# Kernel optimization log

Hardware: AMD Instinct MI355X
Metric: run time of the kernel (lower is better)

## Reference

```python
import jax, jax.numpy as jnp
import numpy as np

HID = 4544; NH = 71; NKV = 1; HD = 64  # Falcon-7B MQA geometry (head_dim hardcoded 64 in _split_heads)
B = 1; U = 32; C = 4; S = 2048          # batch, users, kv chunks, chunk length


def rotate_half(x):
    d = x.shape[-1] // 2
    return jnp.concatenate((-x[..., d:], x[..., :d]), axis=-1)


def setup_inputs() -> dict:
    key = jax.random.key(0)
    ks = jax.random.split(key, 7)
    hidden_states = jax.random.normal(ks[0], (B, U, HID), jnp.float32)
    cos = jax.random.uniform(ks[1], (1, U, 1, HD), jnp.float32, -1.0, 1.0)
    sin = jax.random.uniform(ks[2], (1, U, 1, HD), jnp.float32, -1.0, 1.0)
    k_cache = jax.random.normal(ks[3], (C, B, U, S, HD), jnp.float32)
    v_cache = jax.random.normal(ks[4], (C, B, U, S, HD), jnp.float32)
    attn_masks = jnp.zeros((C, B, U, S), jnp.float32)
    w_qkv = jax.random.normal(ks[5], ((NKV * (NH // NKV + 2)) * HD, HID), jnp.float32) * 0.02
    w_dense = jax.random.normal(ks[6], (HID, HID), jnp.float32) * 0.02
    return {"hidden_states": hidden_states, "cos": cos, "sin": sin,
            "k_cache": k_cache, "v_cache": v_cache, "attn_masks": attn_masks,
            "w_qkv": w_qkv, "w_dense": w_dense}


def reference(hidden_states, cos, sin, k_cache, v_cache, attn_masks, w_qkv, w_dense):
    b, u, _ = hidden_states.shape
    # fused QKV projection (Linear without bias: x @ W.T)
    fused = hidden_states @ w_qkv.T                      # [b,u,(NH+2*NKV)*HD]
    qkv = fused.reshape(b, u, NKV, NH // NKV + 2, HD)    # _split_heads view
    q = qkv[:, :, :, :-2].reshape(b, u, NH, HD)          # query heads
    k_cur = qkv[:, :, :, -2].reshape(b, u, NKV, HD)      # shared MQA key head
    v_cur = qkv[:, :, :, -1].reshape(b, u, NKV, HD)      # shared MQA value head
    # rotary embedding (apply_rotary_pos_emb)
    q = q * cos + rotate_half(q) * sin
    k_cur = k_cur * cos + rotate_half(k_cur) * sin
    inv = 1.0 / jnp.sqrt(jnp.float32(HD))
    # flash-decode over cached chunks: scores [c,b,u,n,s]
    scores = jnp.einsum('bund,cbusd->cbuns', q, k_cache) * inv
    scores = scores + attn_masks[:, :, :, None, :]
    m_c = jnp.max(scores, axis=-1, keepdims=True)        # [c,b,u,n,1] local max
    p = jnp.exp(scores - m_c)
    l_c = jnp.sum(p, axis=-1, keepdims=True)             # local row sums
    # current token = length-1 chunk (its local max is itself, local sum is 1)
    s_cur = jnp.einsum('bund,bued->bune', q, k_cur) * inv  # [b,u,n,1]
    g = jnp.maximum(jnp.max(m_c, axis=0), s_cur)           # global max [b,u,n,1]
    factor = jnp.exp(m_c - g[None])                        # per-chunk rescale
    out = jnp.einsum('cbuns,cbusd->bund', factor * p, v_cache)
    cur_w = jnp.exp(s_cur - g)                             # [b,u,n,1]
    out = out + cur_w * v_cur                              # v_cur broadcasts over heads
    scale = jnp.sum(factor * l_c, axis=0) + cur_w
    out = out / scale
    attn = out.reshape(b, u, NH * HD)
    return attn @ w_dense.T
```

## Files before the change

### kernel.cpp

```cpp
#include <hip/hip_runtime.h>
#include <hip/hip_bf16.h>

typedef __bf16 bf16_t;
typedef __bf16 bf16x8 __attribute__((ext_vector_type(8)));
typedef float  f32x4  __attribute__((ext_vector_type(4)));

#define MFMA16(A,B,C) __builtin_amdgcn_mfma_f32_16x16x32_bf16(A,B,C,0,0,0)

constexpr int HIDc = 4544;
constexpr int NHc  = 71;
constexpr int NHPc = 80;
constexpr int HDc  = 64;
constexpr int Uc   = 32;
constexpr int Sc   = 2048;
constexpr int RQ   = 4672;

constexpr size_t OFF_FUSED = 0;
constexpr size_t OFF_QHI   = 598016;
constexpr size_t OFF_QLO   = 925696;
constexpr size_t OFF_KCUR  = 1253376;
constexpr size_t OFF_VCUR  = 1261568;
constexpr size_t OFF_MP    = 1269760;
constexpr size_t OFF_LP    = 1415168;
constexpr size_t OFF_AHI   = 1560576;
constexpr size_t OFF_ALO   = 1851392;
constexpr size_t OFF_OP    = 2142208;

__device__ __forceinline__ bf16x8 ld8f(const float* base, long eidx) {
  const float* p = base + eidx;
  const f32x4 a = *(const f32x4*)p;
  const f32x4 b = *(const f32x4*)(p + 4);
  bf16x8 r;
  r[0]=(bf16_t)a[0]; r[1]=(bf16_t)a[1]; r[2]=(bf16_t)a[2]; r[3]=(bf16_t)a[3];
  r[4]=(bf16_t)b[0]; r[5]=(bf16_t)b[1]; r[6]=(bf16_t)b[2]; r[7]=(bf16_t)b[3];
  return r;
}

__device__ __forceinline__ void cp16(const float* g, float* l) {
  __builtin_amdgcn_global_load_lds((const __attribute__((address_space(1))) void*)g,
                                   (__attribute__((address_space(3))) void*)l, 16, 0, 0);
}
__device__ __forceinline__ void cp4(const float* g, float* l) {
  __builtin_amdgcn_global_load_lds((const __attribute__((address_space(1))) void*)g,
                                   (__attribute__((address_space(3))) void*)l, 4, 0, 0);
}

__global__ __launch_bounds__(256) void k_zeros(float* fused, float* out) {
  const int i = blockIdx.x*256 + threadIdx.x;
  if (i < Uc*RQ) fused[i] = 0.f;
  else           out[i - Uc*RQ] = 0.f;
}

__global__ __launch_bounds__(256) void k_qkv(
    const float* __restrict__ hidden, const float* __restrict__ wqkv,
    float* __restrict__ fused)
{
  const int h = blockIdx.x, y = blockIdx.y;
  const int t = threadIdx.x;
  const int wave = t >> 6, lane = t & 63;
  const int c = lane & 15, q4 = lane >> 4;
  const int mt = wave & 1, kh = wave >> 1;
  const int ks0 = y*18;
  const int ksn = min(18, 142 - ks0);
  const int h1  = ksn >> 1;
  const int kbeg = ks0 + (kh ? h1 : 0);
  const int kend = ks0 + (kh ? ksn : h1);
  __shared__ float sD[Uc*HDc];

  const long abase = (long)(mt*16 + c)*HIDc + q4*8;
  const long bbase = ((long)h*64 + c)*HIDc + q4*8;
  f32x4 acc[4] = {};
#pragma unroll 3
  for (int ks = kbeg; ks < kend; ++ks) {
    const bf16x8 af = ld8f(hidden, abase + ks*32);
#pragma unroll
    for (int nf = 0; nf < 4; ++nf) {
      const bf16x8 bv = ld8f(wqkv, bbase + (long)nf*16*HIDc + ks*32);
      acc[nf] = MFMA16(af, bv, acc[nf]);
    }
  }
  if (kh == 0) {
#pragma unroll
    for (int r = 0; r < 4; ++r)
#pragma unroll
      for (int nf = 0; nf < 4; ++nf)
        sD[(mt*16 + q4*4 + r)*64 + nf*16 + c] = acc[nf][r];
  }
  __syncthreads();
  if (kh == 1) {
#pragma unroll
    for (int r = 0; r < 4; ++r)
#pragma unroll
      for (int nf = 0; nf < 4; ++nf)
        sD[(mt*16 + q4*4 + r)*64 + nf*16 + c] += acc[nf][r];
  }
  __syncthreads();
  for (int i = t; i < Uc*HDc; i += 256)
    atomicAdd(&fused[(long)(i >> 6)*RQ + h*64 + (i & 63)], sD[i]);
}

__global__ __launch_bounds__(256) void k_rotary(
    const float* __restrict__ fused,
    const float* __restrict__ cosp, const float* __restrict__ sinp,
    bf16_t* __restrict__ qhi, bf16_t* __restrict__ qlo,
    float* __restrict__ kcur, float* __restrict__ vcur)
{
  const int h = blockIdx.x;
  const int t = threadIdx.x;
  __shared__ float sD[Uc*HDc];
  if (h < 73) {
    for (int i = t; i < Uc*HDc; i += 256)
      sD[i] = fused[(long)(i >> 6)*RQ + h*64 + (i & 63)];
    __syncthreads();
  }
  if (h >= NHc) {
    for (int i = t; i < Uc*HDc; i += 256) {
      const long idx = (((long)(i >> 6))*NHPc + h)*HDc + (i & 63);
      qhi[idx] = (bf16_t)0.f;  qlo[idx] = (bf16_t)0.f;
    }
  }
  if (h >= 73) return;
  for (int i = t; i < Uc*HDc; i += 256) {
    const int u = i >> 6, d = i & 63;
    const float x = sD[i];
    const float partner = sD[i ^ 32];
    const float cs = cosp[u*HDc + d];
    const float sn = sinp[u*HDc + d];
    const float rh = (d < 32) ? -partner : partner;
    const float val = x*cs + rh*sn;
    if (h < NHc) {
      const long idx = ((long)u*NHPc + h)*HDc + d;
      const bf16_t hi = (bf16_t)val;
      qhi[idx] = hi;
      qlo[idx] = (bf16_t)(val - (float)hi);
    } else if (h == NHc) {
      kcur[u*HDc + d] = val;
    } else {
      vcur[u*HDc + d] = x;
    }
  }
}

constexpr int ATTN_SMEM_FLOATS = 35456;
constexpr int ATTN_SMEM_BYTES  = ATTN_SMEM_FLOATS * 4;

__global__ __launch_bounds__(256, 1) void k_attn(
    const float* __restrict__ kc, const float* __restrict__ vc,
    const float* __restrict__ masks,
    const bf16_t* __restrict__ qhi, const bf16_t* __restrict__ qlo,
    float* __restrict__ Mp, float* __restrict__ Lp, float* __restrict__ Op,
    const int NPB)
{
  extern __shared__ float smem[];
  const int u  = blockIdx.x;
  const int pb = blockIdx.y;
  const int tid = threadIdx.x;
  const int wave = __builtin_amdgcn_readfirstlane(tid >> 6);
  const int lane = tid & 63;
  const int c    = lane & 15;
  const int q4   = lane >> 4;
  const int pbpc = NPB >> 2;
  const int keys_pb   = 2048 / pbpc;
  const int keys_wave = keys_pb >> 2;
  const int tcnt      = keys_wave >> 5;
  const int chunk = pb / pbpc;
  const int inner = pb - chunk*pbpc;
  const int s_base = inner*keys_pb + wave*keys_wave;
  const long kvbase = ((long)(chunk*Uc + u))*Sc;

  float* const wstage = smem + wave*8192;
  float* const mwave  = smem + 32768 + wave*512;
  float* const sM     = smem + 34816;
  float* const sL     = smem + 35136;
  float* const sO     = smem;

  const int srow = lane >> 4;
  const int scol = (lane & 15) << 2;

  {
    const long tb = (kvbase + s_base) * 64;
    const float* gK = kc + tb;
    const float* gV = vc + tb;
#pragma unroll
    for (int i = 0; i < 8; ++i) {
      const int row = i*4 + srow;
      const int fz = ((row & 7) << 2) ^ (((row >> 3) & 1) << 4);
      const int off = row*64 + (scol ^ fz);
      cp16(gK + off, wstage + i*256);
      cp16(gV + off, wstage + 2048 + i*256);
    }
    const int nmc = keys_wave >> 6;
    const float* gM = masks + kvbase + s_base;
    for (int i = 0; i < nmc; ++i)
      cp4(gM + i*64 + lane, mwave + i*64);
  }

  bf16x8 qh[5][2], ql[5][2];
  const bf16_t* qb  = qhi + ((long)u*NHPc + c)*HDc + q4*8;
  const bf16_t* qb2 = qlo + ((long)u*NHPc + c)*HDc + q4*8;
#pragma unroll
  for (int ht = 0; ht < 5; ++ht)
#pragma unroll
    for (int ks = 0; ks < 2; ++ks) {
      qh[ht][ks] = *(const bf16x8*)(qb  + ht*16*HDc + ks*32);
      ql[ht][ks] = *(const bf16x8*)(qb2 + ht*16*HDc + ks*32);
    }

  float m_i[5], l_i[5];
  f32x4 Oa[5][4] = {};
#pragma unroll
  for (int ht = 0; ht < 5; ++ht) { m_i[ht] = -INFINITY; l_i[ht] = 0.f; }

  const int krow0 = ((c >> 2) << 3) + (c & 3);

  for (int t = 0; t < tcnt; ++t) {
    float* const lK = wstage + (t & 1)*4096;
    float* const lV = lK + 2048;

    if (t + 1 < tcnt) {
      float* const nK = wstage + ((t+1) & 1)*4096;
      const long tb = (kvbase + s_base + (long)(t+1)*32) * 64;
      const float* gK = kc + tb;
      const float* gV = vc + tb;
#pragma unroll
      for (int i = 0; i < 8; ++i) {
        const int row = i*4 + srow;
        const int fz = ((row & 7) << 2) ^ (((row >> 3) & 1) << 4);
        const int off = row*64 + (scol ^ fz);
        cp16(gK + off, nK + i*256);
        cp16(gV + off, nK + 2048 + i*256);
      }
      asm volatile("s_waitcnt vmcnt(16)" ::: "memory");
    } else {
      asm volatile("s_waitcnt vmcnt(0)" ::: "memory");
    }
    __builtin_amdgcn_sched_barrier(0);

    bf16x8 kf[2][2];
#pragma unroll
    for (int mt2 = 0; mt2 < 2; ++mt2) {
      const int row = krow0 + mt2*4;
      const int fz = ((row & 7) << 2) ^ (((row >> 3) & 1) << 4);
#pragma unroll
      for (int ks = 0; ks < 2; ++ks) {
        const int b0 = row*64 + ((ks*32 + q4*8) ^ fz);
        const int b1 = row*64 + ((ks*32 + q4*8 + 4) ^ fz);
        const f32x4 a = *(const f32x4*)(lK + b0);
        const f32x4 b = *(const f32x4*)(lK + b1);
        bf16x8 r;
        r[0]=(bf16_t)a[0]; r[1]=(bf16_t)a[1]; r[2]=(bf16_t)a[2]; r[3]=(bf16_t)a[3];
        r[4]=(bf16_t)b[0]; r[5]=(bf16_t)b[1]; r[6]=(bf16_t)b[2]; r[7]=(bf16_t)b[3];
        kf[mt2][ks] = r;
      }
    }

    bf16x8 vf[4];
#pragma unroll
    for (int dt = 0; dt < 4; ++dt) {
      union { bf16_t e[8]; bf16x8 v; } uv;
#pragma unroll
      for (int j = 0; j < 8; ++j) {
        const int row = q4*8 + j;
        const int fz = ((row & 7) << 2) ^ (((row >> 3) & 1) << 4);
        uv.e[j] = (bf16_t)lV[row*64 + ((dt*16 + c) ^ fz)];
      }
      vf[dt] = uv.v;
    }

    f32x4 S[2][5];
#pragma unroll
    for (int mt2 = 0; mt2 < 2; ++mt2)
#pragma unroll
      for (int ht = 0; ht < 5; ++ht) {
        f32x4 s = {};
        s = MFMA16(kf[mt2][0], qh[ht][0], s);
        s = MFMA16(kf[mt2][1], qh[ht][1], s);
        s = MFMA16(kf[mt2][0], ql[ht][0], s);
        s = MFMA16(kf[mt2][1], ql[ht][1], s);
        S[mt2][ht] = s;
      }

    float mk[2][4];
#pragma unroll
    for (int mt2 = 0; mt2 < 2; ++mt2)
#pragma unroll
      for (int r = 0; r < 4; ++r)
        mk[mt2][r] = mwave[t*32 + q4*8 + mt2*4 + r];
#pragma unroll
    for (int mt2 = 0; mt2 < 2; ++mt2)
#pragma unroll
      for (int ht = 0; ht < 5; ++ht)
#pragma unroll
        for (int r = 0; r < 4; ++r)
          S[mt2][ht][r] = S[mt2][ht][r]*0.125f + mk[mt2][r];

    float alpha[5];
#pragma unroll
    for (int ht = 0; ht < 5; ++ht) {
      float tm = S[0][ht][0];
#pragma unroll
      for (int mt2 = 0; mt2 < 2; ++mt2)
#pragma unroll
        for (int r = 0; r < 4; ++r) tm = fmaxf(tm, S[mt2][ht][r]);
      tm = fmaxf(tm, __shfl_xor(tm, 16));
      tm = fmaxf(tm, __shfl_xor(tm, 32));
      const float mn = fmaxf(m_i[ht], tm);
      alpha[ht] = __expf(m_i[ht] - mn);
      m_i[ht] = mn;
    }
#pragma unroll
    for (int mt2 = 0; mt2 < 2; ++mt2)
#pragma unroll
      for (int ht = 0; ht < 5; ++ht)
#pragma unroll
        for (int r = 0; r < 4; ++r)
          S[mt2][ht][r] = __expf(S[mt2][ht][r] - m_i[ht]);
#pragma unroll
    for (int ht = 0; ht < 5; ++ht) {
      float rs = 0.f;
#pragma unroll
      for (int mt2 = 0; mt2 < 2; ++mt2)
#pragma unroll
        for (int r = 0; r < 4; ++r) rs += S[mt2][ht][r];
      rs += __shfl_xor(rs, 16);
      rs += __shfl_xor(rs, 32);
      l_i[ht] = l_i[ht]*alpha[ht] + rs;
    }
#pragma unroll
    for (int ht = 0; ht < 5; ++ht)
#pragma unroll
      for (int r = 0; r < 4; ++r) {
        const float ar = __shfl(alpha[ht], q4*4 + r);
#pragma unroll
        for (int dt = 0; dt < 4; ++dt) Oa[ht][dt][r] *= ar;
      }
    bf16x8 ph[5], pl[5];
#pragma unroll
    for (int ht = 0; ht < 5; ++ht) {
      union { bf16_t e[8]; bf16x8 v; } uh, ul;
#pragma unroll
      for (int j = 0; j < 8; ++j) {
        const float val = (j < 4) ? S[0][ht][j] : S[1][ht][j & 3];
        const bf16_t hi = (bf16_t)val;
        uh.e[j] = hi;
        ul.e[j] = (bf16_t)(val - (float)hi);
      }
      ph[ht] = uh.v;  pl[ht] = ul.v;
    }
#pragma unroll
    for (int ht = 0; ht < 5; ++ht)
#pragma unroll
      for (int dt = 0; dt < 4; ++dt) {
        Oa[ht][dt] = MFMA16(ph[ht], vf[dt], Oa[ht][dt]);
        Oa[ht][dt] = MFMA16(pl[ht], vf[dt], Oa[ht][dt]);
      }
  }

  if (lane < 16)
#pragma unroll
    for (int ht = 0; ht < 5; ++ht) {
      sM[wave*80 + ht*16 + lane] = m_i[ht];
      sL[wave*80 + ht*16 + lane] = l_i[ht];
    }
  __syncthreads();
#pragma unroll
  for (int ht = 0; ht < 5; ++ht)
#pragma unroll
    for (int r = 0; r < 4; ++r) {
      const int hh = ht*16 + q4*4 + r;
      float mg = fmaxf(fmaxf(sM[hh], sM[80 + hh]), fmaxf(sM[160 + hh], sM[240 + hh]));
      mg = fmaxf(mg, -1e30f);
      const float aw = __expf(sM[wave*80 + hh] - mg);
#pragma unroll
      for (int dt = 0; dt < 4; ++dt) Oa[ht][dt][r] *= aw;
    }
  for (int w = 0; w < 4; ++w) {
    if (wave == w) {
#pragma unroll
      for (int ht = 0; ht < 5; ++ht)
#pragma unroll
        for (int dt = 0; dt < 4; ++dt)
#pragma unroll
          for (int r = 0; r < 4; ++r) {
            const int idx = (ht*16 + q4*4 + r)*HDc + dt*16 + c;
            if (w == 0) sO[idx] = Oa[ht][dt][r];
            else        sO[idx] += Oa[ht][dt][r];
          }
    }
    __syncthreads();
  }
  float* op = Op + ((long)u*NPB + pb)*NHc*HDc;
  for (int i = tid; i < NHc*HDc; i += 256) op[i] = sO[i];
  if (wave == 0 && lane < 16) {
#pragma unroll
    for (int ht = 0; ht < 5; ++ht) {
      const int hh = ht*16 + lane;
      if (hh < NHc) {
        float mg = fmaxf(fmaxf(sM[hh], sM[80 + hh]), fmaxf(sM[160 + hh], sM[240 + hh]));
        mg = fmaxf(mg, -1e30f);
        float L = 0.f;
#pragma unroll
        for (int w = 0; w < 4; ++w) L += __expf(sM[w*80 + hh] - mg)*sL[w*80 + hh];
        Mp[((long)u*NPB + pb)*NHc + hh] = mg;
        Lp[((long)u*NPB + pb)*NHc + hh] = L;
      }
    }
  }
}

__global__ __launch_bounds__(64) void k_combine(
    const float* __restrict__ Mp, const float* __restrict__ Lp,
    const float* __restrict__ Op,
    const bf16_t* __restrict__ qhi, const bf16_t* __restrict__ qlo,
    const float* __restrict__ kcur, const float* __restrict__ vcur,
    bf16_t* __restrict__ ahi, bf16_t* __restrict__ alo, const int NPB)
{
  const int h = blockIdx.x, u = blockIdx.y;
  const int lane = threadIdx.x;
  const long qidx = ((long)u*NHPc + h)*HDc + lane;
  float pr = ((float)qhi[qidx] + (float)qlo[qidx]) * kcur[u*HDc + lane];
#pragma unroll
  for (int o = 32; o > 0; o >>= 1) pr += __shfl_xor(pr, o);
  const float s_cur = pr * 0.125f;

  float g = s_cur;
  for (int p = 0; p < NPB; ++p)
    g = fmaxf(g, Mp[((long)u*NPB + p)*NHc + h]);
  g = fmaxf(g, -1e30f);
  float sw = 0.f, acc = 0.f;
  const float* ob = Op + (long)u*NPB*NHc*HDc + (long)h*HDc + lane;
  for (int p = 0; p < NPB; ++p) {
    const float f = __expf(Mp[((long)u*NPB + p)*NHc + h] - g);
    sw += f*Lp[((long)u*NPB + p)*NHc + h];
    acc += f*ob[(long)p*NHc*HDc];
  }
  const float cw = __expf(s_cur - g);
  acc += cw * vcur[u*HDc + lane];
  const float attn = acc / (sw + cw);
  const bf16_t hi = (bf16_t)attn;
  ahi[(long)u*HIDc + h*HDc + lane] = hi;
  alo[(long)u*HIDc + h*HDc + lane] = (bf16_t)(attn - (float)hi);
}

__global__ __launch_bounds__(256) void k_outgemm(
    const bf16_t* __restrict__ ahi, const bf16_t* __restrict__ alo,
    const float* __restrict__ wd, float* __restrict__ out)
{
  const int nb = blockIdx.x, y = blockIdx.y;
  const int t = threadIdx.x;
  const int wave = t >> 6, lane = t & 63;
  const int c = lane & 15, q4 = lane >> 4;
  const int mt = wave & 1, kh = wave >> 1;
  const int ks0 = y*18;
  const int ksn = min(18, 142 - ks0);
  const int h1  = ksn >> 1;
  const int kbeg = ks0 + (kh ? h1 : 0);
  const int kend = ks0 + (kh ? ksn : h1);
  __shared__ float sC[Uc*32];

  const bf16_t* aph = ahi + ((long)(mt*16 + c))*HIDc + q4*8;
  const bf16_t* apl = alo + ((long)(mt*16 + c))*HIDc + q4*8;
  const long bbase = ((long)nb*32 + c)*HIDc + q4*8;

  f32x4 acc[2] = {};
#pragma unroll 3
  for (int ks = kbeg; ks < kend; ++ks) {
    const bf16x8 Ah = *(const bf16x8*)(aph + ks*32);
    const bf16x8 Al = *(const bf16x8*)(apl + ks*32);
#pragma unroll
    for (int nf = 0; nf < 2; ++nf) {
      const bf16x8 B = ld8f(wd, bbase + (long)nf*16*HIDc + ks*32);
      acc[nf] = MFMA16(Ah, B, acc[nf]);
      acc[nf] = MFMA16(Al, B, acc[nf]);
    }
  }
  if (kh == 0) {
#pragma unroll
    for (int r = 0; r < 4; ++r)
#pragma unroll
      for (int nf = 0; nf < 2; ++nf)
        sC[(mt*16 + q4*4 + r)*32 + nf*16 + c] = acc[nf][r];
  }
  __syncthreads();
  if (kh == 1) {
#pragma unroll
    for (int r = 0; r < 4; ++r)
#pragma unroll
      for (int nf = 0; nf < 2; ++nf)
        sC[(mt*16 + q4*4 + r)*32 + nf*16 + c] += acc[nf][r];
  }
  __syncthreads();
  for (int i = t; i < Uc*32; i += 256)
    atomicAdd(&out[(long)(i >> 5)*HIDc + nb*32 + (i & 31)], sC[i]);
}

extern "C" void kernel_launch(void* const* d_in, const int* in_sizes, int n_in,
                              void* d_out, int out_size, void* d_ws, size_t ws_size,
                              hipStream_t stream)
{
  const float* hidden = (const float*)d_in[0];
  const float* cosp   = (const float*)d_in[1];
  const float* sinp   = (const float*)d_in[2];
  const float* kcache = (const float*)d_in[3];
  const float* vcache = (const float*)d_in[4];
  const float* masks  = (const float*)d_in[5];
  const float* wqkv   = (const float*)d_in[6];
  const float* wdense = (const float*)d_in[7];
  float* out = (float*)d_out;

  const size_t opb = (size_t)Uc*NHc*HDc*4;
  int NPB = 16;
  if      (ws_size >= OFF_OP + 16*opb) NPB = 16;
  else if (ws_size >= OFF_OP +  8*opb) NPB = 8;
  else if (ws_size >= OFF_OP +  4*opb) NPB = 4;
  else return;

  char* ws = (char*)d_ws;
  float*  fused = (float*)(ws + OFF_FUSED);
  bf16_t* qhi   = (bf16_t*)(ws + OFF_QHI);
  bf16_t* qlo   = (bf16_t*)(ws + OFF_QLO);
  float*  kcur  = (float*)(ws + OFF_KCUR);
  float*  vcur  = (float*)(ws + OFF_VCUR);
  float*  Mp    = (float*)(ws + OFF_MP);
  float*  Lp    = (float*)(ws + OFF_LP);
  bf16_t* ahi   = (bf16_t*)(ws + OFF_AHI);
  bf16_t* alo   = (bf16_t*)(ws + OFF_ALO);
  float*  Op    = (float*)(ws + OFF_OP);

  hipFuncSetAttribute(reinterpret_cast<const void*>(k_attn),
                      hipFuncAttributeMaxDynamicSharedMemorySize, ATTN_SMEM_BYTES);

  k_zeros  <<<1152, 256, 0, stream>>>(fused, out);
  k_qkv    <<<dim3(73, 8), 256, 0, stream>>>(hidden, wqkv, fused);
  k_rotary <<<80, 256, 0, stream>>>(fused, cosp, sinp, qhi, qlo, kcur, vcur);
  k_attn   <<<dim3(32, NPB), 256, ATTN_SMEM_BYTES, stream>>>(kcache, vcache, masks, qhi, qlo, Mp, Lp, Op, NPB);
  k_combine<<<dim3(71, 32), 64, 0, stream>>>(Mp, Lp, Op, qhi, qlo, kcur, vcur, ahi, alo, NPB);
  k_outgemm<<<dim3(142, 8), 256, 0, stream>>>(ahi, alo, wdense, out);
}
```

Baseline: 353.7 us.

## Warp-specialize attention: producer waves stream K/V, consumer waves own one head tile

The attention kernel moves to 512 threads. Three producer waves load K, V and the mask into a shared 4-slot ring buffer, while five consumer waves each handle one 16-head tile over all keys in the block. Because every consumer sees the full key range, the cross-wave softmax merge and the shared-memory reduction of O are gone. In return, each K/V tile is read from LDS and converted to bf16 five times instead of once, and every tile step needs two block-wide barriers. The return path of the producer waves relies on the raw s_barrier count matching __syncthreads in the consumers, which is fragile.

```diff
diff --git a/kernel.cpp b/kernel.cpp
--- a/kernel.cpp
+++ b/kernel.cpp
@@ -141,10 +141,12 @@
   }
 }
 
-constexpr int ATTN_SMEM_FLOATS = 35456;
-constexpr int ATTN_SMEM_BYTES  = ATTN_SMEM_FLOATS * 4;
-
-__global__ __launch_bounds__(256, 1) void k_attn(
+constexpr int ATTN_SLOT_F   = 4096;
+constexpr int ATTN_STAGE_F  = 4*ATTN_SLOT_F;
+constexpr int ATTN_SMEM_F   = ATTN_STAGE_F + 2048;
+constexpr int ATTN_SMEM_BYTES = ATTN_SMEM_F * 4;
+
+__global__ __launch_bounds__(512, 4) void k_attn(
     const float* __restrict__ kc, const float* __restrict__ vc,
     const float* __restrict__ masks,
     const bf16_t* __restrict__ qhi, const bf16_t* __restrict__ qlo,
@@ -160,81 +162,88 @@
   const int c    = lane & 15;
   const int q4   = lane >> 4;
   const int pbpc = NPB >> 2;
-  const int keys_pb   = 2048 / pbpc;
-  const int keys_wave = keys_pb >> 2;
-  const int tcnt      = keys_wave >> 5;
+  const int keys_pb = 2048 / pbpc;
+  const int tcnt    = keys_pb >> 5;
   const int chunk = pb / pbpc;
   const int inner = pb - chunk*pbpc;
-  const int s_base = inner*keys_pb + wave*keys_wave;
+  const int s_base = inner*keys_pb;
   const long kvbase = ((long)(chunk*Uc + u))*Sc;
 
-  float* const wstage = smem + wave*8192;
-  float* const mwave  = smem + 32768 + wave*512;
-  float* const sM     = smem + 34816;
-  float* const sL     = smem + 35136;
-  float* const sO     = smem;
+  float* const stage = smem;
+  float* const smask = smem + ATTN_STAGE_F;
 
   const int srow = lane >> 4;
   const int scol = (lane & 15) << 2;
 
-  {
-    const long tb = (kvbase + s_base) * 64;
-    const float* gK = kc + tb;
-    const float* gV = vc + tb;
-#pragma unroll
-    for (int i = 0; i < 8; ++i) {
-      const int row = i*4 + srow;
-      const int fz = ((row & 7) << 2) ^ (((row >> 3) & 1) << 4);
-      const int off = row*64 + (scol ^ fz);
-      cp16(gK + off, wstage + i*256);
-      cp16(gV + off, wstage + 2048 + i*256);
-    }
-    const int nmc = keys_wave >> 6;
-    const float* gM = masks + kvbase + s_base;
-    for (int i = 0; i < nmc; ++i)
-      cp4(gM + i*64 + lane, mwave + i*64);
-  }
-
-  bf16x8 qh[5][2], ql[5][2];
-  const bf16_t* qb  = qhi + ((long)u*NHPc + c)*HDc + q4*8;
-  const bf16_t* qb2 = qlo + ((long)u*NHPc + c)*HDc + q4*8;
-#pragma unroll
-  for (int ht = 0; ht < 5; ++ht)
-#pragma unroll
-    for (int ks = 0; ks < 2; ++ks) {
-      qh[ht][ks] = *(const bf16x8*)(qb  + ht*16*HDc + ks*32);
-      ql[ht][ks] = *(const bf16x8*)(qb2 + ht*16*HDc + ks*32);
-    }
-
-  float m_i[5], l_i[5];
-  f32x4 Oa[5][4] = {};
-#pragma unroll
-  for (int ht = 0; ht < 5; ++ht) { m_i[ht] = -INFINITY; l_i[ht] = 0.f; }
-
-  const int krow0 = ((c >> 2) << 3) + (c & 3);
-
-  for (int t = 0; t < tcnt; ++t) {
-    float* const lK = wstage + (t & 1)*4096;
-    float* const lV = lK + 2048;
-
-    if (t + 1 < tcnt) {
-      float* const nK = wstage + ((t+1) & 1)*4096;
-      const long tb = (kvbase + s_base + (long)(t+1)*32) * 64;
-      const float* gK = kc + tb;
-      const float* gV = vc + tb;
+  if (wave >= 5) {
+    if (wave == 7) {
+      const int nmc = keys_pb >> 6;
+      const float* gM = masks + kvbase + s_base;
+      for (int i = 0; i < nmc; ++i)
+        cp4(gM + i*64 + lane, smask + i*64);
+      for (int t = 0; t < tcnt; ++t) {
+        __builtin_amdgcn_s_barrier();
+        if (t == 0) asm volatile("s_waitcnt vmcnt(0)" ::: "memory");
+        __builtin_amdgcn_s_barrier();
+      }
+      return;
+    }
+    const float* gsrc = (wave == 5) ? kc : vc;
+    const int vofs = (wave == 6) ? 2048 : 0;
+    for (int pt = 0; pt < 3; ++pt) {
+      const long tb = (kvbase + s_base + pt*32) * 64;
+      float* dst = stage + pt*ATTN_SLOT_F + vofs;
 #pragma unroll
       for (int i = 0; i < 8; ++i) {
         const int row = i*4 + srow;
         const int fz = ((row & 7) << 2) ^ (((row >> 3) & 1) << 4);
-        const int off = row*64 + (scol ^ fz);
-        cp16(gK + off, nK + i*256);
-        cp16(gV + off, nK + 2048 + i*256);
-      }
-      asm volatile("s_waitcnt vmcnt(16)" ::: "memory");
-    } else {
-      asm volatile("s_waitcnt vmcnt(0)" ::: "memory");
-    }
-    __builtin_amdgcn_sched_barrier(0);
+        cp16(gsrc + tb + row*64 + (scol ^ fz), dst + i*256);
+      }
+    }
+    for (int t = 0; t < tcnt; ++t) {
+      __builtin_amdgcn_s_barrier();
+      if (t + 3 < tcnt) {
+        const long tb = (kvbase + s_base + (long)(t+3)*32) * 64;
+        float* dst = stage + ((t+3)&3)*ATTN_SLOT_F + vofs;
+#pragma unroll
+        for (int i = 0; i < 8; ++i) {
+          const int row = i*4 + srow;
+          const int fz = ((row & 7) << 2) ^ (((row >> 3) & 1) << 4);
+          cp16(gsrc + tb + row*64 + (scol ^ fz), dst + i*256);
+        }
+      }
+      const int rem = min(3, tcnt - 1 - t);
+      if      (rem >= 3) asm volatile("s_waitcnt vmcnt(24)" ::: "memory");
+      else if (rem == 2) asm volatile("s_waitcnt vmcnt(16)" ::: "memory");
+      else if (rem == 1) asm volatile("s_waitcnt vmcnt(8)"  ::: "memory");
+      else               asm volatile("s_waitcnt vmcnt(0)"  ::: "memory");
+      __builtin_amdgcn_s_barrier();
+    }
+    return;
+  }
+
+  const int ht = wave;
+  bf16x8 qh[2], ql[2];
+  {
+    const bf16_t* qb  = qhi + ((long)u*NHPc + ht*16 + c)*HDc + q4*8;
+    const bf16_t* qb2 = qlo + ((long)u*NHPc + ht*16 + c)*HDc + q4*8;
+#pragma unroll
+    for (int ks = 0; ks < 2; ++ks) {
+      qh[ks] = *(const bf16x8*)(qb  + ks*32);
+      ql[ks] = *(const bf16x8*)(qb2 + ks*32);
+    }
+  }
+
+  float m_i = -INFINITY, l_i = 0.f;
+  f32x4 Oa[4] = {};
+
+  const int krow0 = ((c >> 2) << 3) + (c & 3);
+
+  for (int t = 0; t < tcnt; ++t) {
+    __syncthreads();
+    __syncthreads();
+    float* const lK = stage + (t & 3)*ATTN_SLOT_F;
+    float* const lV = lK + 2048;
 
     bf16x8 kf[2][2];
 #pragma unroll
@@ -267,143 +276,85 @@
       vf[dt] = uv.v;
     }
 
-    f32x4 S[2][5];
+    f32x4 S[2];
+#pragma unroll
+    for (int mt2 = 0; mt2 < 2; ++mt2) {
+      f32x4 s = {};
+      s = MFMA16(kf[mt2][0], qh[0], s);
+      s = MFMA16(kf[mt2][1], qh[1], s);
+      s = MFMA16(kf[mt2][0], ql[0], s);
+      s = MFMA16(kf[mt2][1], ql[1], s);
+      S[mt2] = s;
+    }
+
 #pragma unroll
     for (int mt2 = 0; mt2 < 2; ++mt2)
 #pragma unroll
-      for (int ht = 0; ht < 5; ++ht) {
-        f32x4 s = {};
-        s = MFMA16(kf[mt2][0], qh[ht][0], s);
-        s = MFMA16(kf[mt2][1], qh[ht][1], s);
-        s = MFMA16(kf[mt2][0], ql[ht][0], s);
-        s = MFMA16(kf[mt2][1], ql[ht][1], s);
-        S[mt2][ht] = s;
-      }
-
-    float mk[2][4];
+      for (int r = 0; r < 4; ++r)
+        S[mt2][r] = S[mt2][r]*0.125f + smask[t*32 + q4*8 + mt2*4 + r];
+
+    float tm = S[0][0];
 #pragma unroll
     for (int mt2 = 0; mt2 < 2; ++mt2)
 #pragma unroll
+      for (int r = 0; r < 4; ++r) tm = fmaxf(tm, S[mt2][r]);
+    tm = fmaxf(tm, __shfl_xor(tm, 16));
+    tm = fmaxf(tm, __shfl_xor(tm, 32));
+    const float mn = fmaxf(m_i, tm);
+    const float alpha = __expf(m_i - mn);
+    m_i = mn;
+#pragma unroll
+    for (int mt2 = 0; mt2 < 2; ++mt2)
+#pragma unroll
       for (int r = 0; r < 4; ++r)
-        mk[mt2][r] = mwave[t*32 + q4*8 + mt2*4 + r];
+        S[mt2][r] = __expf(S[mt2][r] - m_i);
+    float rs = 0.f;
 #pragma unroll
     for (int mt2 = 0; mt2 < 2; ++mt2)
 #pragma unroll
-      for (int ht = 0; ht < 5; ++ht)
-#pragma unroll
-        for (int r = 0; r < 4; ++r)
-          S[mt2][ht][r] = S[mt2][ht][r]*0.125f + mk[mt2][r];
-
-    float alpha[5];
-#pragma unroll
-    for (int ht = 0; ht < 5; ++ht) {
-      float tm = S[0][ht][0];
-#pragma unroll
-      for (int mt2 = 0; mt2 < 2; ++mt2)
-#pragma unroll
-        for (int r = 0; r < 4; ++r) tm = fmaxf(tm, S[mt2][ht][r]);
-      tm = fmaxf(tm, __shfl_xor(tm, 16));
-      tm = fmaxf(tm, __shfl_xor(tm, 32));
-      const float mn = fmaxf(m_i[ht], tm);
-      alpha[ht] = __expf(m_i[ht] - mn);
-      m_i[ht] = mn;
-    }
-#pragma unroll
-    for (int mt2 = 0; mt2 < 2; ++mt2)
-#pragma unroll
-      for (int ht = 0; ht < 5; ++ht)
-#pragma unroll
-        for (int r = 0; r < 4; ++r)
-          S[mt2][ht][r] = __expf(S[mt2][ht][r] - m_i[ht]);
-#pragma unroll
-    for (int ht = 0; ht < 5; ++ht) {
-      float rs = 0.f;
-#pragma unroll
-      for (int mt2 = 0; mt2 < 2; ++mt2)
-#pragma unroll
-        for (int r = 0; r < 4; ++r) rs += S[mt2][ht][r];
-      rs += __shfl_xor(rs, 16);
-      rs += __shfl_xor(rs, 32);
-      l_i[ht] = l_i[ht]*alpha[ht] + rs;
-    }
-#pragma unroll
-    for (int ht = 0; ht < 5; ++ht)
-#pragma unroll
-      for (int r = 0; r < 4; ++r) {
-        const float ar = __shfl(alpha[ht], q4*4 + r);
-#pragma unroll
-        for (int dt = 0; dt < 4; ++dt) Oa[ht][dt][r] *= ar;
-      }
-    bf16x8 ph[5], pl[5];
-#pragma unroll
-    for (int ht = 0; ht < 5; ++ht) {
+      for (int r = 0; r < 4; ++r) rs += S[mt2][r];
+    rs += __shfl_xor(rs, 16);
+    rs += __shfl_xor(rs, 32);
+    l_i = l_i*alpha + rs;
+
+#pragma unroll
+    for (int r = 0; r < 4; ++r) {
+      const float ar = __shfl(alpha, q4*4 + r);
+#pragma unroll
+      for (int dt = 0; dt < 4; ++dt) Oa[dt][r] *= ar;
+    }
+    bf16x8 ph, pl;
+    {
       union { bf16_t e[8]; bf16x8 v; } uh, ul;
 #pragma unroll
       for (int j = 0; j < 8; ++j) {
-        const float val = (j < 4) ? S[0][ht][j] : S[1][ht][j & 3];
+        const float val = (j < 4) ? S[0][j] : S[1][j & 3];
         const bf16_t hi = (bf16_t)val;
         uh.e[j] = hi;
         ul.e[j] = (bf16_t)(val - (float)hi);
       }
-      ph[ht] = uh.v;  pl[ht] = ul.v;
-    }
-#pragma unroll
-    for (int ht = 0; ht < 5; ++ht)
-#pragma unroll
-      for (int dt = 0; dt < 4; ++dt) {
-        Oa[ht][dt] = MFMA16(ph[ht], vf[dt], Oa[ht][dt]);
-        Oa[ht][dt] = MFMA16(pl[ht], vf[dt], Oa[ht][dt]);
-      }
-  }
-
-  if (lane < 16)
-#pragma unroll
-    for (int ht = 0; ht < 5; ++ht) {
-      sM[wave*80 + ht*16 + lane] = m_i[ht];
-      sL[wave*80 + ht*16 + lane] = l_i[ht];
-    }
-  __syncthreads();
-#pragma unroll
-  for (int ht = 0; ht < 5; ++ht)
+      ph = uh.v;  pl = ul.v;
+    }
+#pragma unroll
+    for (int dt = 0; dt < 4; ++dt) {
+      Oa[dt] = MFMA16(ph, vf[dt], Oa[dt]);
+      Oa[dt] = MFMA16(pl, vf[dt], Oa[dt]);
+    }
+  }
+
+  float* op = Op + ((long)u*NPB + pb)*NHc*HDc;
+#pragma unroll
+  for (int dt = 0; dt < 4; ++dt)
 #pragma unroll
     for (int r = 0; r < 4; ++r) {
-      const int hh = ht*16 + q4*4 + r;
-      float mg = fmaxf(fmaxf(sM[hh], sM[80 + hh]), fmaxf(sM[160 + hh], sM[240 + hh]));
-      mg = fmaxf(mg, -1e30f);
-      const float aw = __expf(sM[wave*80 + hh] - mg);
-#pragma unroll
-      for (int dt = 0; dt < 4; ++dt) Oa[ht][dt][r] *= aw;
-    }
-  for (int w = 0; w < 4; ++w) {
-    if (wave == w) {
-#pragma unroll
-      for (int ht = 0; ht < 5; ++ht)
-#pragma unroll
-        for (int dt = 0; dt < 4; ++dt)
-#pragma unroll
-          for (int r = 0; r < 4; ++r) {
-            const int idx = (ht*16 + q4*4 + r)*HDc + dt*16 + c;
-            if (w == 0) sO[idx] = Oa[ht][dt][r];
-            else        sO[idx] += Oa[ht][dt][r];
-          }
-    }
-    __syncthreads();
-  }
-  float* op = Op + ((long)u*NPB + pb)*NHc*HDc;
-  for (int i = tid; i < NHc*HDc; i += 256) op[i] = sO[i];
-  if (wave == 0 && lane < 16) {
-#pragma unroll
-    for (int ht = 0; ht < 5; ++ht) {
-      const int hh = ht*16 + lane;
-      if (hh < NHc) {
-        float mg = fmaxf(fmaxf(sM[hh], sM[80 + hh]), fmaxf(sM[160 + hh], sM[240 + hh]));
-        mg = fmaxf(mg, -1e30f);
-        float L = 0.f;
-#pragma unroll
-        for (int w = 0; w < 4; ++w) L += __expf(sM[w*80 + hh] - mg)*sL[w*80 + hh];
-        Mp[((long)u*NPB + pb)*NHc + hh] = mg;
-        Lp[((long)u*NPB + pb)*NHc + hh] = L;
-      }
+      const int h = ht*16 + q4*4 + r;
+      if (h < NHc) op[h*HDc + dt*16 + c] = Oa[dt][r];
+    }
+  if (q4 == 0) {
+    const int hh = ht*16 + c;
+    if (hh < NHc) {
+      Mp[((long)u*NPB + pb)*NHc + hh] = fmaxf(m_i, -1e30f);
+      Lp[((long)u*NPB + pb)*NHc + hh] = l_i;
     }
   }
 }
@@ -533,7 +484,7 @@
   k_zeros  <<<1152, 256, 0, stream>>>(fused, out);
   k_qkv    <<<dim3(73, 8), 256, 0, stream>>>(hidden, wqkv, fused);
   k_rotary <<<80, 256, 0, stream>>>(fused, cosp, sinp, qhi, qlo, kcur, vcur);
-  k_attn   <<<dim3(32, NPB), 256, ATTN_SMEM_BYTES, stream>>>(kcache, vcache, masks, qhi, qlo, Mp, Lp, Op, NPB);
+  k_attn   <<<dim3(32, NPB), 512, ATTN_SMEM_BYTES, stream>>>(kcache, vcache, masks, qhi, qlo, Mp, Lp, Op, NPB);
   k_combine<<<dim3(71, 32), 64, 0, stream>>>(Mp, Lp, Op, qhi, qlo, kcur, vcur, ahi, alo, NPB);
   k_outgemm<<<dim3(142, 8), 256, 0, stream>>>(ahi, alo, wdense, out);
 }
```

After: 334.7 us. -5.4%, faster.
